# Performance work log

Hardware: AMD Instinct MI355X
Metric: run time of the kernel (lower is better)

Reference implementation:

```python
import jax, jax.numpy as jnp
import numpy as np

DIM_MEMORY = 64
NUM_SLOTS = 131072
SHIFT_RADIUS = 1
D_IN = 256
BATCH = 256
EPS = 1e-8


def setup_inputs() -> dict:
    key = jax.random.key(0)
    k1, k2, k3, k4 = jax.random.split(key, 4)
    d_out = DIM_MEMORY + 1 + 1 + (2 * SHIFT_RADIUS + 1) + 1 + 1  # = 70
    return {
        "input_from_controller": jax.random.normal(k1, (BATCH, D_IN), dtype=jnp.float32),
        "memory": jax.random.normal(k2, (NUM_SLOTS, DIM_MEMORY), dtype=jnp.float32),
        "previous_weighting": jax.random.uniform(k3, (BATCH, NUM_SLOTS), dtype=jnp.float32),
        "W": jax.random.normal(k4, (D_IN, d_out), dtype=jnp.float32) * (1.0 / np.sqrt(D_IN)),
        "b": jnp.zeros((d_out,), dtype=jnp.float32),
    }


def _ntm_head(input_from_controller, memory, previous_weighting, W, b):
    M, R = DIM_MEMORY, SHIFT_RADIUS
    K = 2 * R + 1
    combined = input_from_controller @ W + b  # [B, 70]
    key_vector = combined[:, :M]                       # [B, M]
    key_strength = combined[:, M:M + 1]                # [B, 1]
    gate = jax.nn.sigmoid(combined[:, M + 1:M + 2])    # [B, 1]
    conv_kernel = jax.nn.softmax(combined[:, M + 2:M + 2 + K], axis=1)  # [B, K]
    # sharpening_factor = relu(...) + 1 is computed in the original but never
    # used in the returned value, so it is dead code and omitted here.

    # content addressing: cosine similarity of key against every memory slot
    dots = jnp.einsum("bm,nm->bn", key_vector, memory)          # [B, N]
    key_norm = jnp.linalg.norm(key_vector, axis=1, keepdims=True)  # [B, 1]
    mem_norm = jnp.linalg.norm(memory, axis=1)                     # [N]
    cos = dots / (key_norm * mem_norm[None, :] + EPS)
    w_c = jax.nn.softmax(cos * key_strength, axis=-1)            # [B, N]

    # interpolation gate
    w_g = w_c * gate + (1.0 - gate) * previous_weighting         # [B, N]

    # circular shift convolution: w_s[i] = sum_k w_g[(i - 1 + k) % N] * kernel[k]
    N = w_g.shape[1]
    idx = (jnp.arange(N)[:, None] - 1 + jnp.arange(K)[None, :]) % N  # [N, K]
    w_s = jnp.einsum("bnk,bk->bn", w_g[:, idx], conv_kernel)        # [B, N]
    return w_s


def reference(input_from_controller, memory, previous_weighting, W, b):
    return _ntm_head(input_from_controller, memory, previous_weighting, W, b)
```

## Files before the change

### kernel.cpp

```cpp
#include <hip/hip_runtime.h>

#define NSLOTS 131072
#define NMASK  (NSLOTS-1)
#define NBATCH 256
#define DMEM   64
#define DIN    256
#define DCOMB  71
#define SPB    64
#define NBLK   (NSLOTS/SPB)
#define EPSF   1e-8f

typedef unsigned int   u32;
typedef unsigned short u16;
typedef __bf16 bf16x8 __attribute__((ext_vector_type(8)));
typedef float  f32x4  __attribute__((ext_vector_type(4)));

__device__ __forceinline__ u16 f2bf(float f) {
  u32 u = __builtin_bit_cast(u32, f);
  u += 0x7fffu + ((u >> 16) & 1u);
  return (u16)(u >> 16);
}
__device__ __forceinline__ float bf2f(u16 v) {
  return __builtin_bit_cast(float, ((u32)v) << 16);
}
__device__ __forceinline__ u32 pk2(float a, float b) {
  return (u32)f2bf(a) | ((u32)f2bf(b) << 16);
}
__device__ __forceinline__ float blo(u32 u){ return __builtin_bit_cast(float, u << 16); }
__device__ __forceinline__ float bhi(u32 u){ return __builtin_bit_cast(float, u & 0xffff0000u); }

__global__ __launch_bounds__(128) void ntm_prep(
    const float* __restrict__ inp, const float* __restrict__ W,
    const float* __restrict__ bias, u16* __restrict__ keysbf,
    float* __restrict__ params)
{
  __shared__ float comb[DCOMB];
  const int b = blockIdx.x;
  const int t = threadIdx.x;
  if (t < DCOMB) {
    float acc = bias[t];
    const float* ip = inp + (size_t)b * DIN;
    for (int i = 0; i < DIN; ++i) acc = fmaf(ip[i], W[i*DCOMB + t], acc);
    comb[t] = acc;
  }
  __syncthreads();
  if (t < 64) {
    float k = comb[t];
    keysbf[b*64 + t] = f2bf(k);
    float sq = k * k;
#pragma unroll
    for (int d = 1; d < 64; d <<= 1) sq += __shfl_xor(sq, d, 64);
    if (t == 0) {
      float kn = sqrtf(sq);
      float ks = comb[64];
      params[b*8+0] = ks / kn;
      params[b*8+1] = fabsf(ks);
      params[b*8+2] = 1.f/(1.f + __expf(-comb[65]));
      float c0 = comb[66], c1 = comb[67], c2 = comb[68];
      float mx = fmaxf(c0, fmaxf(c1, c2));
      float e0 = __expf(c0-mx), e1 = __expf(c1-mx), e2 = __expf(c2-mx);
      float inv = 1.f/(e0+e1+e2);
      params[b*8+3] = e0*inv; params[b*8+4] = e1*inv; params[b*8+5] = e2*inv;
    }
  }
}

__global__ __launch_bounds__(512, 6) void ntm_dots(
    const u16* __restrict__ keysbf, const float* __restrict__ memory,
    const float* __restrict__ params, u16* __restrict__ ug,
    float* __restrict__ sumpart)
{
  __shared__ __align__(16) u16 pool[128*128];
  __shared__ __align__(16) u16 meml[128*DMEM];
  __shared__ float invmn[128];
  const int t     = threadIdx.x;
  const int bbase = blockIdx.x * 128;
  const int s0    = blockIdx.y * 128;

  {
    const int r = t >> 3, c8 = t & 7;
#pragma unroll
    for (int h = 0; h < 2; ++h) {
      int rr = r + h*64;
      const float* mp = memory + (size_t)(s0 + rr) * DMEM + c8 * 8;
      float4 f0 = *(const float4*)mp;
      float4 f1 = *(const float4*)(mp + 4);
      uint4 v;
      v.x = pk2(f0.x, f0.y); v.y = pk2(f0.z, f0.w);
      v.z = pk2(f1.x, f1.y); v.w = pk2(f1.z, f1.w);
      *(uint4*)&meml[rr*DMEM + ((c8 ^ (rr & 7)) << 3)] = v;
      float sq = f0.x*f0.x + f0.y*f0.y + f0.z*f0.z + f0.w*f0.w
               + f1.x*f1.x + f1.y*f1.y + f1.z*f1.z + f1.w*f1.w;
      sq += __shfl_xor(sq, 1, 64);
      sq += __shfl_xor(sq, 2, 64);
      sq += __shfl_xor(sq, 4, 64);
      if (c8 == 0) invmn[rr] = rsqrtf(sq);
    }
  }
  __syncthreads();

  const int w = t >> 6, L = t & 63;
  const int li = L & 15, hi4 = L >> 4;
  const int bb = bbase + w*16 + li;
  const int pb = w*16 + li;
  const uint4* kb = (const uint4*)(keysbf + (size_t)bb * DMEM);
  const float abk = params[bb*8+0];
  const float C   = params[bb*8+1];

  f32x4 zero = {0.f, 0.f, 0.f, 0.f};
  f32x4 acc[8];
#pragma unroll
  for (int rt = 0; rt < 8; ++rt) acc[rt] = zero;

#pragma unroll
  for (int ks = 0; ks < 2; ++ks) {
    int cb = ks*4 + hi4;
    bf16x8 bfr = __builtin_bit_cast(bf16x8, kb[cb]);
#pragma unroll
    for (int rt = 0; rt < 8; ++rt) {
      int rr = rt*16 + li;
      bf16x8 af = __builtin_bit_cast(bf16x8, *(const uint4*)&meml[rr*DMEM + ((cb ^ (rr&7)) << 3)]);
      acc[rt] = __builtin_amdgcn_mfma_f32_16x16x32_bf16(af, bfr, acc[rt], 0, 0, 0);
    }
  }

  float s_acc = 0.f;
#pragma unroll
  for (int rt = 0; rt < 8; ++rt) {
    int sbase = rt*16 + hi4*4;
    float wv[4];
#pragma unroll
    for (int r = 0; r < 4; ++r)
      wv[r] = __expf(acc[rt][r] * abk * invmn[sbase + r] - C);
    s_acc += wv[0] + wv[1] + wv[2] + wv[3];
    uint2 pkd;
    pkd.x = pk2(wv[0], wv[1]);
    pkd.y = pk2(wv[2], wv[3]);
    int chunk = rt*4 + hi4;
    int cs = chunk ^ (pb & 31);
    *(uint2*)&pool[pb*128 + cs*4] = pkd;
  }
  s_acc += __shfl_xor(s_acc, 16, 64);
  s_acc += __shfl_xor(s_acc, 32, 64);
  if (hi4 == 0) sumpart[(size_t)bb*1024 + blockIdx.y] = s_acc;
  __syncthreads();

#pragma unroll
  for (int p = 0; p < 2; ++p) {
    int row = p*64 + (t >> 3);
    int seg = t & 7;
    uint2 wu[4];
#pragma unroll
    for (int j = 0; j < 4; ++j) {
      int c = seg*4 + j;
      int cs = c ^ (row & 31);
      wu[j] = *(const uint2*)&pool[row*128 + cs*4];
    }
    uint4 v0, v1;
    v0.x = wu[0].x; v0.y = wu[0].y; v0.z = wu[1].x; v0.w = wu[1].y;
    v1.x = wu[2].x; v1.y = wu[2].y; v1.z = wu[3].x; v1.w = wu[3].y;
    uint4* dst = (uint4*)(ug + (size_t)(bbase + row) * NSLOTS + s0 + seg*16);
    dst[0] = v0; dst[1] = v1;
  }
}

__global__ __launch_bounds__(256) void ntm_reduce(
    const float* __restrict__ sumpart, float* __restrict__ Sv, int nparts)
{
  __shared__ float red[4];
  const int b = blockIdx.x, t = threadIdx.x;
  const int w = t >> 6, L = t & 63;
  float s = 0.f;
  for (int i = t; i < nparts; i += 256) s += sumpart[(size_t)b*nparts + i];
#pragma unroll
  for (int d = 1; d < 64; d <<= 1) s += __shfl_xor(s, d, 64);
  if (L == 0) red[w] = s;
  __syncthreads();
  if (t == 0) Sv[b] = red[0] + red[1] + red[2] + red[3];
}

__global__ __launch_bounds__(256, 8) void ntm_conv(
    const u16* __restrict__ ug, const float* __restrict__ params,
    const float* __restrict__ Sv, const float* __restrict__ prev,
    float* __restrict__ out)
{
  const int b    = blockIdx.y;
  const int t    = threadIdx.x;
  const int so   = blockIdx.x * 1024 + t * 4;
  const int L    = t & 63;
  const float gg  = params[b*8+2];
  const float c0f = params[b*8+3], c1f = params[b*8+4], c2f = params[b*8+5];
  const float og  = 1.f - gg;
  const float gs  = gg / Sv[b];
  const float* pv = prev + (size_t)b * NSLOTS;
  const u16*   uv = ug   + (size_t)b * NSLOTS;
  float*       ov = out  + (size_t)b * NSLOTS;

  f32x4 p = __builtin_nontemporal_load((const f32x4*)(pv + so));
  uint2 uu = *(const uint2*)(uv + so);
  float f0 = fmaf(og, p.x, gs * blo(uu.x));
  float f1 = fmaf(og, p.y, gs * bhi(uu.x));
  float f2 = fmaf(og, p.z, gs * blo(uu.y));
  float f3 = fmaf(og, p.w, gs * bhi(uu.y));

  float fl = __shfl_up(f3, 1, 64);
  float fr = __shfl_down(f0, 1, 64);
  if (L == 0) {
    int sm = (so - 1) & NMASK;
    fl = fmaf(og, pv[sm], gs * bf2f(uv[sm]));
  }
  if (L == 63) {
    int sp = (so + 4) & NMASK;
    fr = fmaf(og, pv[sp], gs * bf2f(uv[sp]));
  }

  f32x4 o;
  o.x = c0f*fl + c1f*f0 + c2f*f1;
  o.y = c0f*f0 + c1f*f1 + c2f*f2;
  o.z = c0f*f1 + c1f*f2 + c2f*f3;
  o.w = c0f*f2 + c1f*f3 + c2f*fr;
  __builtin_nontemporal_store(o, (f32x4*)(ov + so));
}

__global__ __launch_bounds__(512, 8) void ntm_stats_fb(
    const u16* __restrict__ keysbf, const float* __restrict__ memory,
    const float* __restrict__ params, float* __restrict__ sumpart)
{
  __shared__ __align__(16) u16 meml[SPB*DMEM];
  __shared__ float invmn[SPB];
  const int t     = threadIdx.x;
  const int s0    = blockIdx.x * SPB;
  const int bbase = blockIdx.y * 128;
  {
    int r = t >> 3, c8 = t & 7;
    const float* mp = memory + (size_t)(s0 + r) * DMEM + c8 * 8;
    float4 f0 = *(const float4*)mp;
    float4 f1 = *(const float4*)(mp + 4);
    uint4 v;
    v.x = pk2(f0.x, f0.y); v.y = pk2(f0.z, f0.w);
    v.z = pk2(f1.x, f1.y); v.w = pk2(f1.z, f1.w);
    *(uint4*)&meml[r*DMEM + ((c8 ^ (r & 7)) << 3)] = v;
    float sq = f0.x*f0.x + f0.y*f0.y + f0.z*f0.z + f0.w*f0.w
             + f1.x*f1.x + f1.y*f1.y + f1.z*f1.z + f1.w*f1.w;
    sq += __shfl_xor(sq, 1, 64);
    sq += __shfl_xor(sq, 2, 64);
    sq += __shfl_xor(sq, 4, 64);
    if (c8 == 0) invmn[r] = rsqrtf(sq);
  }
  __syncthreads();
  const int w = t >> 6, L = t & 63;
  const int li = L & 15, hi4 = L >> 4;
  const int bb = bbase + w*16 + li;
  const uint4* kb = (const uint4*)(keysbf + (size_t)bb * DMEM);
  f32x4 zero = {0.f, 0.f, 0.f, 0.f};
  f32x4 acc[4];
#pragma unroll
  for (int rt = 0; rt < 4; ++rt) acc[rt] = zero;
#pragma unroll
  for (int ks = 0; ks < 2; ++ks) {
    int cb = ks*4 + hi4;
    bf16x8 bfr = __builtin_bit_cast(bf16x8, kb[cb]);
#pragma unroll
    for (int rt = 0; rt < 4; ++rt) {
      int r = rt*16 + li;
      bf16x8 af = __builtin_bit_cast(bf16x8, *(const uint4*)&meml[r*DMEM + ((cb ^ (r&7)) << 3)]);
      acc[rt] = __builtin_amdgcn_mfma_f32_16x16x32_bf16(af, bfr, acc[rt], 0, 0, 0);
    }
  }
  float abk = params[bb*8 + 0];
  float C   = params[bb*8 + 1];
  float s = 0.f;
#pragma unroll
  for (int rt = 0; rt < 4; ++rt)
#pragma unroll
    for (int r = 0; r < 4; ++r) {
      int sl = rt*16 + hi4*4 + r;
      s += __expf(acc[rt][r] * abk * invmn[sl] - C);
    }
  s += __shfl_xor(s, 16, 64);
  s += __shfl_xor(s, 32, 64);
  if (hi4 == 0) sumpart[(size_t)bb*NBLK + blockIdx.x] = s;
}

__global__ __launch_bounds__(512, 8) void ntm_final_fb(
    const u16* __restrict__ keysbf, const float* __restrict__ memory,
    const float* __restrict__ params, const float* __restrict__ Sv,
    const float* __restrict__ prev, float* __restrict__ out)
{
  __shared__ __align__(16) u16 pool[128*DMEM];
  __shared__ __align__(16) u16 meml[SPB*DMEM];
  __shared__ __align__(16) u16 halom[2*DMEM];
  __shared__ float invmn[SPB];
  __shared__ float invhn[2];
  __shared__ u16 hlo[128], hhi[128];
  const int t     = threadIdx.x;
  const int s0    = blockIdx.x * SPB;
  const int bbase = blockIdx.y * 128;
  {
    int r = t >> 3, c8 = t & 7;
    const float* mp = memory + (size_t)(s0 + r) * DMEM + c8 * 8;
    float4 f0 = *(const float4*)mp;
    float4 f1 = *(const float4*)(mp + 4);
    uint4 v;
    v.x = pk2(f0.x, f0.y); v.y = pk2(f0.z, f0.w);
    v.z = pk2(f1.x, f1.y); v.w = pk2(f1.z, f1.w);
    *(uint4*)&meml[r*DMEM + ((c8 ^ (r & 7)) << 3)] = v;
    float sq = f0.x*f0.x + f0.y*f0.y + f0.z*f0.z + f0.w*f0.w
             + f1.x*f1.x + f1.y*f1.y + f1.z*f1.z + f1.w*f1.w;
    sq += __shfl_xor(sq, 1, 64);
    sq += __shfl_xor(sq, 2, 64);
    sq += __shfl_xor(sq, 4, 64);
    if (c8 == 0) invmn[r] = rsqrtf(sq);
  }
  if (t < 128) {
    int h = t >> 6, m = t & 63;
    int gs = (s0 + (h ? SPB : -1)) & NMASK;
    float v = memory[(size_t)gs * DMEM + m];
    halom[h*DMEM + m] = f2bf(v);
    float sq = v * v;
#pragma unroll
    for (int d = 1; d < 64; d <<= 1) sq += __shfl_xor(sq, d, 64);
    if (m == 0) invhn[h] = rsqrtf(sq);
  }
  __syncthreads();
  const int w = t >> 6, L = t & 63;
  const int li = L & 15, hi4 = L >> 4;
  const int bb = bbase + w*16 + li;
  const int pb = w*16 + li;
  const uint4* kb = (const uint4*)(keysbf + (size_t)bb * DMEM);
  f32x4 zero = {0.f, 0.f, 0.f, 0.f};
  f32x4 acc[4];
#pragma unroll
  for (int rt = 0; rt < 4; ++rt) acc[rt] = zero;
#pragma unroll
  for (int ks = 0; ks < 2; ++ks) {
    int cb = ks*4 + hi4;
    bf16x8 bfr = __builtin_bit_cast(bf16x8, kb[cb]);
#pragma unroll
    for (int rt = 0; rt < 4; ++rt) {
      int r = rt*16 + li;
      bf16x8 af = __builtin_bit_cast(bf16x8, *(const uint4*)&meml[r*DMEM + ((cb ^ (r&7)) << 3)]);
      acc[rt] = __builtin_amdgcn_mfma_f32_16x16x32_bf16(af, bfr, acc[rt], 0, 0, 0);
    }
  }
  if (t < 256) {
    int hb = t & 127, hh = t >> 7;
    int gb = bbase + hb;
    const uint4* kb2 = (const uint4*)(keysbf + (size_t)gb * DMEM);
    float dot = 0.f;
#pragma unroll
    for (int mb = 0; mb < 8; ++mb) {
      uint4 kv = kb2[mb];
      uint4 mv = *(const uint4*)&halom[hh*DMEM + mb*8];
      dot += blo(kv.x)*blo(mv.x) + bhi(kv.x)*bhi(mv.x);
      dot += blo(kv.y)*blo(mv.y) + bhi(kv.y)*bhi(mv.y);
      dot += blo(kv.z)*blo(mv.z) + bhi(kv.z)*bhi(mv.z);
      dot += blo(kv.w)*blo(mv.w) + bhi(kv.w)*bhi(mv.w);
    }
    float abk2 = params[gb*8+0], C2 = params[gb*8+1], gg2 = params[gb*8+2];
    float l = dot * abk2 * invhn[hh];
    u16 hv = f2bf(__expf(l - C2) * gg2 / Sv[gb]);
    if (hh) hhi[hb] = hv; else hlo[hb] = hv;
  }
  {
    float abk = params[bb*8+0], C = params[bb*8+1], gg = params[bb*8+2];
    float wfac = gg / Sv[bb];
#pragma unroll
    for (int rt = 0; rt < 4; ++rt) {
      int sbase = rt*16 + hi4*4;
      float wv[4];
#pragma unroll
      for (int r = 0; r < 4; ++r) {
        int sl = sbase + r;
        wv[r] = __expf(acc[rt][r] * abk * invmn[sl] - C) * wfac;
      }
      uint2 pkd;
      pkd.x = pk2(wv[0], wv[1]);
      pkd.y = pk2(wv[2], wv[3]);
      *(uint2*)&pool[pb*DMEM + (((sbase >> 2) ^ (pb & 15)) << 2)] = pkd;
    }
  }
  __syncthreads();
  {
    const int g2 = t & 15;
    const int tb = t >> 4;
    const int so = g2 * 4;
#pragma unroll
    for (int p = 0; p < 4; ++p) {
      int pb2 = p*32 + tb;
      int bb2 = bbase + pb2;
      float gg = params[bb2*8+2];
      float c0 = params[bb2*8+3], c1 = params[bb2*8+4], c2 = params[bb2*8+5];
      float og = 1.f - gg;
      const float* pv = prev + (size_t)bb2 * NSLOTS;
      float4 pr = *(const float4*)(pv + s0 + so);
      uint2 wu = *(const uint2*)&pool[pb2*DMEM + ((g2 ^ (pb2 & 15)) << 2)];
      float w0 = blo(wu.x), w1 = bhi(wu.x), w2 = blo(wu.y), w3 = bhi(wu.y);
      float lpr = __shfl_up(pr.w, 1, 64);
      float rpr = __shfl_down(pr.x, 1, 64);
      float lw  = __shfl_up(w3, 1, 64);
      float rw  = __shfl_down(w0, 1, 64);
      if (g2 == 0)  { lpr = pv[(s0 - 1) & NMASK];   lw = bf2f(hlo[pb2]); }
      if (g2 == 15) { rpr = pv[(s0 + SPB) & NMASK]; rw = bf2f(hhi[pb2]); }
      float fm1 = fmaf(og, lpr,  lw);
      float f0  = fmaf(og, pr.x, w0);
      float f1  = fmaf(og, pr.y, w1);
      float f2  = fmaf(og, pr.z, w2);
      float f3  = fmaf(og, pr.w, w3);
      float f4  = fmaf(og, rpr,  rw);
      float4 o;
      o.x = c0*fm1 + c1*f0 + c2*f1;
      o.y = c0*f0  + c1*f1 + c2*f2;
      o.z = c0*f1  + c1*f2 + c2*f3;
      o.w = c0*f2  + c1*f3 + c2*f4;
      *(float4*)(out + (size_t)bb2 * NSLOTS + s0 + so) = o;
    }
  }
}

extern "C" void kernel_launch(void* const* d_in, const int* in_sizes, int n_in,
                              void* d_out, int out_size, void* d_ws, size_t ws_size,
                              hipStream_t stream)
{
  (void)in_sizes; (void)n_in; (void)out_size;
  const float* inp    = (const float*)d_in[0];
  const float* memory = (const float*)d_in[1];
  const float* prev   = (const float*)d_in[2];
  const float* W      = (const float*)d_in[3];
  const float* bias   = (const float*)d_in[4];
  float* out = (float*)d_out;
  char*  ws  = (char*)d_ws;

  u16*   keysbf = (u16*)ws;
  float* params = (float*)(ws + 32768);
  float* Sv     = (float*)(ws + 40960);
  float* sumpart = (float*)(ws + 49152);
  u16*   ug      = (u16*)(ws + 49152 + 1048576);

  const size_t need_new = 49152 + 1048576 + (size_t)NBATCH * NSLOTS * 2u;
  const size_t need_fb  = 49152 + (size_t)NBATCH * NBLK * 4u;

  hipLaunchKernelGGL(ntm_prep, dim3(NBATCH), dim3(128), 0, stream, inp, W, bias, keysbf, params);

  if (ws_size >= need_new) {
    hipLaunchKernelGGL(ntm_dots,   dim3(2, NSLOTS/128), dim3(512), 0, stream,
                       keysbf, memory, params, ug, sumpart);
    hipLaunchKernelGGL(ntm_reduce, dim3(NBATCH), dim3(256), 0, stream, sumpart, Sv, 1024);
    hipLaunchKernelGGL(ntm_conv,   dim3(NSLOTS/1024, NBATCH), dim3(256), 0, stream,
                       ug, params, Sv, prev, out);
  } else {
    float* sp = (ws_size >= need_fb) ? sumpart : out;
    hipLaunchKernelGGL(ntm_stats_fb, dim3(NBLK, 2), dim3(512), 0, stream, keysbf, memory, params, sp);
    hipLaunchKernelGGL(ntm_reduce,   dim3(NBATCH),  dim3(256), 0, stream, sp, Sv, NBLK);
    hipLaunchKernelGGL(ntm_final_fb, dim3(NBLK, 2), dim3(512), 0, stream, keysbf, memory, params, Sv, prev, out);
  }
}
```

Before: 112.6 us.

## Write dots output directly from registers, drop LDS staging pool

The dots kernel no longer stages exp weights in a 32KB shared pool for a transposed, coalesced store. Each lane now writes its 4 packed bf16 values (8 bytes) straight to global memory, and the MFMA tile is processed in two groups of four to cut accumulator registers. The occupancy hint rises from 6 to 8 waves. This removes the LDS round trip and a barrier, but global writes become scattered 8-byte stores across rows instead of 32-byte contiguous segments. The prep GEMV also gains four independent accumulators.

```diff
diff --git a/kernel.cpp b/kernel.cpp
--- a/kernel.cpp
+++ b/kernel.cpp
@@ -38,10 +38,16 @@
   const int b = blockIdx.x;
   const int t = threadIdx.x;
   if (t < DCOMB) {
-    float acc = bias[t];
+    float a0 = 0.f, a1 = 0.f, a2 = 0.f, a3 = 0.f;
     const float* ip = inp + (size_t)b * DIN;
-    for (int i = 0; i < DIN; ++i) acc = fmaf(ip[i], W[i*DCOMB + t], acc);
-    comb[t] = acc;
+#pragma unroll 4
+    for (int i = 0; i < DIN; i += 4) {
+      a0 = fmaf(ip[i+0], W[(i+0)*DCOMB + t], a0);
+      a1 = fmaf(ip[i+1], W[(i+1)*DCOMB + t], a1);
+      a2 = fmaf(ip[i+2], W[(i+2)*DCOMB + t], a2);
+      a3 = fmaf(ip[i+3], W[(i+3)*DCOMB + t], a3);
+    }
+    comb[t] = bias[t] + ((a0 + a1) + (a2 + a3));
   }
   __syncthreads();
   if (t < 64) {
@@ -65,12 +71,11 @@
   }
 }
 
-__global__ __launch_bounds__(512, 6) void ntm_dots(
+__global__ __launch_bounds__(512, 8) void ntm_dots(
     const u16* __restrict__ keysbf, const float* __restrict__ memory,
     const float* __restrict__ params, u16* __restrict__ ug,
     float* __restrict__ sumpart)
 {
-  __shared__ __align__(16) u16 pool[128*128];
   __shared__ __align__(16) u16 meml[128*DMEM];
   __shared__ float invmn[128];
   const int t     = threadIdx.x;
@@ -102,66 +107,45 @@
   const int w = t >> 6, L = t & 63;
   const int li = L & 15, hi4 = L >> 4;
   const int bb = bbase + w*16 + li;
-  const int pb = w*16 + li;
   const uint4* kb = (const uint4*)(keysbf + (size_t)bb * DMEM);
   const float abk = params[bb*8+0];
   const float C   = params[bb*8+1];
+  u16* urow = ug + (size_t)bb * NSLOTS + s0;
 
   f32x4 zero = {0.f, 0.f, 0.f, 0.f};
-  f32x4 acc[8];
-#pragma unroll
-  for (int rt = 0; rt < 8; ++rt) acc[rt] = zero;
-
-#pragma unroll
-  for (int ks = 0; ks < 2; ++ks) {
-    int cb = ks*4 + hi4;
-    bf16x8 bfr = __builtin_bit_cast(bf16x8, kb[cb]);
-#pragma unroll
-    for (int rt = 0; rt < 8; ++rt) {
-      int rr = rt*16 + li;
-      bf16x8 af = __builtin_bit_cast(bf16x8, *(const uint4*)&meml[rr*DMEM + ((cb ^ (rr&7)) << 3)]);
-      acc[rt] = __builtin_amdgcn_mfma_f32_16x16x32_bf16(af, bfr, acc[rt], 0, 0, 0);
-    }
-  }
-
   float s_acc = 0.f;
-#pragma unroll
-  for (int rt = 0; rt < 8; ++rt) {
-    int sbase = rt*16 + hi4*4;
-    float wv[4];
-#pragma unroll
-    for (int r = 0; r < 4; ++r)
-      wv[r] = __expf(acc[rt][r] * abk * invmn[sbase + r] - C);
-    s_acc += wv[0] + wv[1] + wv[2] + wv[3];
-    uint2 pkd;
-    pkd.x = pk2(wv[0], wv[1]);
-    pkd.y = pk2(wv[2], wv[3]);
-    int chunk = rt*4 + hi4;
-    int cs = chunk ^ (pb & 31);
-    *(uint2*)&pool[pb*128 + cs*4] = pkd;
+
+#pragma unroll
+  for (int grp = 0; grp < 2; ++grp) {
+    f32x4 acc[4] = {zero, zero, zero, zero};
+#pragma unroll
+    for (int ks = 0; ks < 2; ++ks) {
+      int cb = ks*4 + hi4;
+      bf16x8 bfr = __builtin_bit_cast(bf16x8, kb[cb]);
+#pragma unroll
+      for (int rt4 = 0; rt4 < 4; ++rt4) {
+        int rr = (grp*4 + rt4)*16 + li;
+        bf16x8 af = __builtin_bit_cast(bf16x8, *(const uint4*)&meml[rr*DMEM + ((cb ^ (rr&7)) << 3)]);
+        acc[rt4] = __builtin_amdgcn_mfma_f32_16x16x32_bf16(af, bfr, acc[rt4], 0, 0, 0);
+      }
+    }
+#pragma unroll
+    for (int rt4 = 0; rt4 < 4; ++rt4) {
+      int sbase = (grp*4 + rt4)*16 + hi4*4;
+      float wv[4];
+#pragma unroll
+      for (int r = 0; r < 4; ++r)
+        wv[r] = __expf(acc[rt4][r] * abk * invmn[sbase + r] - C);
+      s_acc += (wv[0] + wv[1]) + (wv[2] + wv[3]);
+      uint2 pkd;
+      pkd.x = pk2(wv[0], wv[1]);
+      pkd.y = pk2(wv[2], wv[3]);
+      *(uint2*)(urow + sbase) = pkd;
+    }
   }
   s_acc += __shfl_xor(s_acc, 16, 64);
   s_acc += __shfl_xor(s_acc, 32, 64);
   if (hi4 == 0) sumpart[(size_t)bb*1024 + blockIdx.y] = s_acc;
-  __syncthreads();
-
-#pragma unroll
-  for (int p = 0; p < 2; ++p) {
-    int row = p*64 + (t >> 3);
-    int seg = t & 7;
-    uint2 wu[4];
-#pragma unroll
-    for (int j = 0; j < 4; ++j) {
-      int c = seg*4 + j;
-      int cs = c ^ (row & 31);
-      wu[j] = *(const uint2*)&pool[row*128 + cs*4];
-    }
-    uint4 v0, v1;
-    v0.x = wu[0].x; v0.y = wu[0].y; v0.z = wu[1].x; v0.w = wu[1].y;
-    v1.x = wu[2].x; v1.y = wu[2].y; v1.z = wu[3].x; v1.w = wu[3].y;
-    uint4* dst = (uint4*)(ug + (size_t)(bbase + row) * NSLOTS + s0 + seg*16);
-    dst[0] = v0; dst[1] = v1;
-  }
 }
 
 __global__ __launch_bounds__(256) void ntm_reduce(
```

New measurement: 111.2 us. About the same (-1.2%).
